# Optimization experiments

Hardware: AMD Instinct MI355X
Metric: run time of the kernel (lower is better)

Reference implementation:

```python
import jax, jax.numpy as jnp
import numpy as np

B, S, CC, CF, E, H, NH = 16, 1024, 8, 8, 64, 1024, 16
DH = H // NH
VOCAB = 10000
EPS = 1e-5


def layer_norm(x, g, b):
    m = x.mean(-1, keepdims=True)
    v = x.var(-1, keepdims=True)
    return (x - m) / jnp.sqrt(v + EPS) * g + b


def setup_inputs():
    key = jax.random.key(0)
    ks = jax.random.split(key, 30)
    f32 = jnp.float32
    n = lambda k, shp, s=0.02: jax.random.normal(k, shp, f32) * s
    inp = {}
    inp['cate_x'] = jax.random.randint(ks[0], (B, S, CC), 0, VOCAB)
    inp['cont_x'] = jax.random.normal(ks[1], (B, S, CF), f32)
    inp['mask'] = jax.random.randint(ks[2], (B, S), 0, 2)
    # parameters
    inp['emb_table'] = n(ks[3], (VOCAB, E)).at[0].set(0.0)  # padding_idx=0
    inp['cate_W'] = n(ks[4], (CC * E, H)); inp['cate_b'] = jnp.zeros((H,), f32)
    inp['cate_ln_g'] = jnp.ones((H,), f32); inp['cate_ln_b'] = jnp.zeros((H,), f32)
    inp['bn_g'] = jnp.ones((CF,), f32); inp['bn_b'] = jnp.zeros((CF,), f32)
    inp['cont_W'] = n(ks[5], (CF, H)); inp['cont_b'] = jnp.zeros((H,), f32)
    inp['cont_ln_g'] = jnp.ones((H,), f32); inp['cont_ln_b'] = jnp.zeros((H,), f32)
    inp['comb_W'] = n(ks[6], (2 * H, H)); inp['comb_b'] = jnp.zeros((H,), f32)
    inp['comb_ln_g'] = jnp.ones((H,), f32); inp['comb_ln_b'] = jnp.zeros((H,), f32)
    inp['Wq'] = n(ks[7], (H, H)); inp['bq'] = jnp.zeros((H,), f32)
    inp['Wk'] = n(ks[8], (H, H)); inp['bk'] = jnp.zeros((H,), f32)
    inp['Wv'] = n(ks[9], (H, H)); inp['bv'] = jnp.zeros((H,), f32)
    inp['Wo'] = n(ks[10], (H, H)); inp['bo'] = jnp.zeros((H,), f32)
    return inp


def reference(cate_x, cont_x, mask, emb_table, cate_W, cate_b, cate_ln_g, cate_ln_b,
              bn_g, bn_b, cont_W, cont_b, cont_ln_g, cont_ln_b,
              comb_W, comb_b, comb_ln_g, comb_ln_b,
              Wq, bq, Wk, bk, Wv, bv, Wo, bo):
    # categorical path: embed -> flatten cols -> Linear+LN
    cate_emb = emb_table[cate_x].reshape(B, S, CC * E)
    cate_h = layer_norm(cate_emb @ cate_W + cate_b, cate_ln_g, cate_ln_b)
    # continuous path: BatchNorm1d over flattened (B*S, CF) with batch stats
    xf = cont_x.reshape(-1, CF)
    mu = xf.mean(0)
    var = xf.var(0)  # biased, as torch BN normalization
    xn = ((xf - mu) / jnp.sqrt(var + EPS) * bn_g + bn_b).reshape(B, S, CF)
    cont_h = layer_norm(xn @ cont_W + cont_b, cont_ln_g, cont_ln_b)
    # combine: ReLU -> Linear -> LN
    seq = jax.nn.relu(jnp.concatenate([cate_h, cont_h], axis=2))
    x = layer_norm(seq @ comb_W + comb_b, comb_ln_g, comb_ln_b)  # [B,S,H]
    # multi-head attention (dropout is identity in eval)
    Q = (x @ Wq + bq).reshape(B, S, NH, DH)
    K = (x @ Wk + bk).reshape(B, S, NH, DH)
    V = (x @ Wv + bv).reshape(B, S, NH, DH)
    scores = jnp.einsum('bqhd,bkhd->bhqk', Q, K) / np.sqrt(DH).astype(np.float32)
    # faithful to source: mask broadcast over the QUERY axis
    scores = jnp.where(mask[:, None, :, None] == 0, -1e7, scores)
    attn = jax.nn.softmax(scores, axis=-1)
    out = jnp.einsum('bhqk,bkhd->bqhd', attn, V).reshape(B, S, H)
    out = out @ Wo + bo
    return out[:, -1:, -1]  # [B,1]
```

## Files before the change

### kernel.cpp

```cpp
#include <hip/hip_runtime.h>
#include <hip/hip_bf16.h>
#include <math.h>

#define EPS 1e-5f

typedef unsigned short u16;
typedef __attribute__((ext_vector_type(8))) short bf16x8;
typedef __attribute__((ext_vector_type(4))) float f32x4;

__device__ __forceinline__ float b2f(u16 u) {
  union { unsigned int i; float f; } v; v.i = ((unsigned int)u) << 16; return v.f;
}
__device__ __forceinline__ u16 f2b(float f) {
  union { float f; unsigned int i; } v; v.f = f;
  unsigned int r = v.i + 0x7fff + ((v.i >> 16) & 1);
  return (u16)(r >> 16);
}

__device__ __forceinline__ void gload_lds16(const u16* g, u16* l) {
  __builtin_amdgcn_global_load_lds(
      (const __attribute__((address_space(1))) unsigned int*)g,
      (__attribute__((address_space(3))) unsigned int*)l, 16, 0, 0);
}

__global__ __launch_bounds__(256) void prep_k(
    const float* __restrict__ cx, float* __restrict__ part_bn,
    float* __restrict__ outacc, float* __restrict__ Sall,
    const float* __restrict__ emb, u16* __restrict__ embb,
    const float* __restrict__ cate_W, u16* __restrict__ cateWT) {
  __shared__ float shmem[64 * 65];
  const int bid = blockIdx.x, tid = threadIdx.x;

  if (bid == 0) {
    if (tid < 16) outacc[tid] = 0.f;
    for (int i = tid; i < 544; i += 256) Sall[i] = 0.f;
    return;
  }
  if (bid <= 64) {
    int pb = bid - 1;
    int gid = pb * 256 + tid;
    float4 a = ((const float4*)cx)[2 * gid];
    float4 b = ((const float4*)cx)[2 * gid + 1];
    float v[16];
    v[0] = a.x; v[1] = a.y; v[2] = a.z; v[3] = a.w;
    v[4] = b.x; v[5] = b.y; v[6] = b.z; v[7] = b.w;
#pragma unroll
    for (int i = 0; i < 8; ++i) v[8 + i] = v[i] * v[i];
#pragma unroll
    for (int off = 32; off; off >>= 1)
#pragma unroll
      for (int i = 0; i < 16; ++i) v[i] += __shfl_down(v[i], off);
    int l = tid & 63, wv_ = tid >> 6;
    if (l == 0)
#pragma unroll
      for (int i = 0; i < 16; ++i) shmem[wv_ * 16 + i] = v[i];
    __syncthreads();
    if (tid < 16)
      part_bn[pb * 16 + tid] = shmem[tid] + shmem[16 + tid] + shmem[32 + tid] + shmem[48 + tid];
    return;
  }
  if (bid <= 689) {
    int i = (bid - 65) * 256 + tid;
    if (i < 160000) {
      float4 v = ((const float4*)emb)[i];
      ushort4 u; u.x = f2b(v.x); u.y = f2b(v.y); u.z = f2b(v.z); u.w = f2b(v.w);
      ((ushort4*)embb)[i] = u;
    }
    return;
  }
  {
    int local = bid - 690;
    int n0 = (local & 15) * 64, k0 = (local >> 4) * 64;
    int c = tid & 63, r0 = tid >> 6;
#pragma unroll
    for (int i = 0; i < 16; ++i) {
      int r = r0 + i * 4;
      shmem[r * 65 + c] = cate_W[(size_t)(k0 + r) * 1024 + n0 + c];
    }
    __syncthreads();
#pragma unroll
    for (int i = 0; i < 16; ++i) {
      int r = r0 + i * 4;
      cateWT[(size_t)(n0 + r) * 512 + k0 + c] = f2b(shmem[c * 65 + r]);
    }
  }
}

template <int MODE>
__global__ __launch_bounds__(512) void gemm256(
    const u16* __restrict__ A0, const u16* __restrict__ A1,
    const int* __restrict__ idx, const u16* __restrict__ embb,
    const u16* __restrict__ BT, const float* __restrict__ bias,
    u16* __restrict__ C, int K) {
  __shared__ u16 As[2][2][8192];
  __shared__ u16 Bs[2][2][8192];
  __shared__ int sidx[MODE == 1 ? 2048 : 4];
  const int tid = threadIdx.x;
  const int bid = blockIdx.x;
  const int chunk = gridDim.x >> 3;
  const int swz = (bid & 7) * chunk + (bid >> 3);
  const int row0 = (swz >> 2) * 256;
  const int col0 = (swz & 3) * 256;

  const int rr8 = tid >> 3;
  const int p8  = tid & 7;
  const int sl  = p8 ^ (rr8 & 7);

  const int l   = tid & 63;
  const int w   = tid >> 6;
  const int wrh = w >> 2;
  const int wcq = w & 3;
  const int hb  = wcq >> 1;
  const int rbb = (wcq & 1) * 64;
  const int lr  = l & 15;
  const int lk  = l >> 4;

  f32x4 acc[8][4];
#pragma unroll
  for (int m = 0; m < 8; ++m)
#pragma unroll
    for (int n = 0; n < 4; ++n) acc[m][n] = (f32x4){0.f, 0.f, 0.f, 0.f};

  const int nt = K >> 6;
  const int nit = nt >> 1;

  if (MODE == 1) {
    *(int4*)&sidx[tid * 4] = *(const int4*)&idx[row0 * 8 + tid * 4];
    __syncthreads();
  }

  auto stageA = [&](int t, int h) {
    const int k0 = t << 6;
    const int buf = t & 1;
#pragma unroll
    for (int i = 0; i < 2; ++i) {
      const u16* asrc;
      if (MODE == 1) {
        int id = sidx[(h * 128 + i * 64 + rr8) * 8 + (k0 >> 6)];
        asrc = embb + (size_t)id * 64 + sl * 8;
      } else {
        int ar = row0 + h * 128 + i * 64 + rr8;
        const u16* base = (k0 < 1024) ? A0 : A1;
        asrc = base + (size_t)ar * 1024 + (k0 & 1023) + sl * 8;
      }
      gload_lds16(asrc, &As[buf][h][i * 4096 + tid * 8]);
    }
  };
  auto stageB = [&](int t, int h) {
    const int k0 = t << 6;
    const int buf = t & 1;
#pragma unroll
    for (int i = 0; i < 2; ++i) {
      int br = col0 + h * 128 + i * 64 + rr8;
      gload_lds16(BT + (size_t)br * K + k0 + sl * 8,
                  &Bs[buf][h][i * 4096 + tid * 8]);
    }
  };

  bf16x8 bfr[4][2];
  auto loadB = [&](int buf) {
#pragma unroll
    for (int n = 0; n < 4; ++n)
#pragma unroll
      for (int ks = 0; ks < 2; ++ks) {
        int rowb = rbb + n * 16 + lr;
        int ph = (ks * 4 + lk) ^ (lr & 7);
        bfr[n][ks] = *(const bf16x8*)&Bs[buf][hb][rowb * 64 + ph * 8];
      }
  };
  auto loadA = [&](bf16x8 (&af)[2][2], int buf, int q) {
#pragma unroll
    for (int mm = 0; mm < 2; ++mm)
#pragma unroll
      for (int ks = 0; ks < 2; ++ks) {
        int rowa = (q * 2 + mm) * 16 + lr;
        int ph = (ks * 4 + lk) ^ (lr & 7);
        af[mm][ks] = *(const bf16x8*)&As[buf][wrh][rowa * 64 + ph * 8];
      }
  };
  auto mfma_quad = [&](bf16x8 (&af)[2][2], int q) {
    __builtin_amdgcn_s_setprio(1);
#pragma unroll
    for (int ks = 0; ks < 2; ++ks)
#pragma unroll
      for (int mm = 0; mm < 2; ++mm)
#pragma unroll
        for (int n = 0; n < 4; ++n)
          acc[q * 2 + mm][n] = __builtin_amdgcn_mfma_f32_16x16x32_bf16(
              af[mm][ks], bfr[n][ks], acc[q * 2 + mm][n], 0, 0, 0);
    __builtin_amdgcn_s_setprio(0);
  };

  stageA(0, 0); stageA(0, 1);
  stageB(0, 0); stageB(0, 1);
  stageB(1, 0); stageB(1, 1);
  asm volatile("s_waitcnt vmcnt(4)" ::: "memory");
  __builtin_amdgcn_s_barrier();

  for (int it = 0; it < nit; ++it) {
    const int T = it * 2;
    const bool more = (T + 2 < nt);
    bf16x8 af[2][2];

    loadB(0); loadA(af, 0, 0);
    stageA(T + 1, 0);
    __builtin_amdgcn_s_barrier();
    asm volatile("s_waitcnt lgkmcnt(0)" ::: "memory");
    mfma_quad(af, 0);
    __builtin_amdgcn_s_barrier();
    loadA(af, 0, 1);
    stageA(T + 1, 1);
    __builtin_amdgcn_s_barrier();
    asm volatile("s_waitcnt lgkmcnt(0)" ::: "memory");
    mfma_quad(af, 1);
    __builtin_amdgcn_s_barrier();
    loadA(af, 0, 2);
    if (more) stageB(T + 2, 0);
    __builtin_amdgcn_s_barrier();
    asm volatile("s_waitcnt lgkmcnt(0)" ::: "memory");
    mfma_quad(af, 2);
    __builtin_amdgcn_s_barrier();
    loadA(af, 0, 3);
    if (more) stageB(T + 2, 1);
    __builtin_amdgcn_s_barrier();
    asm volatile("s_waitcnt lgkmcnt(0)" ::: "memory");
    mfma_quad(af, 3);
    if (more) asm volatile("s_waitcnt vmcnt(4)" ::: "memory");
    else      asm volatile("s_waitcnt vmcnt(0)" ::: "memory");
    __builtin_amdgcn_s_barrier();

    loadB(1); loadA(af, 1, 0);
    if (more) stageA(T + 2, 0);
    __builtin_amdgcn_s_barrier();
    asm volatile("s_waitcnt lgkmcnt(0)" ::: "memory");
    mfma_quad(af, 0);
    __builtin_amdgcn_s_barrier();
    loadA(af, 1, 1);
    if (more) stageA(T + 2, 1);
    __builtin_amdgcn_s_barrier();
    asm volatile("s_waitcnt lgkmcnt(0)" ::: "memory");
    mfma_quad(af, 1);
    __builtin_amdgcn_s_barrier();
    loadA(af, 1, 2);
    if (more) stageB(T + 3, 0);
    __builtin_amdgcn_s_barrier();
    asm volatile("s_waitcnt lgkmcnt(0)" ::: "memory");
    mfma_quad(af, 2);
    __builtin_amdgcn_s_barrier();
    loadA(af, 1, 3);
    if (more) stageB(T + 3, 1);
    __builtin_amdgcn_s_barrier();
    asm volatile("s_waitcnt lgkmcnt(0)" ::: "memory");
    mfma_quad(af, 3);
    if (it + 1 < nit) {
      asm volatile("s_waitcnt vmcnt(4)" ::: "memory");
      __builtin_amdgcn_s_barrier();
    }
  }

  float bv_[4];
#pragma unroll
  for (int n = 0; n < 4; ++n) bv_[n] = bias[col0 + wcq * 64 + n * 16 + lr];
#pragma unroll
  for (int m = 0; m < 8; ++m) {
#pragma unroll
    for (int n = 0; n < 4; ++n) {
      int cc = col0 + wcq * 64 + n * 16 + lr;
#pragma unroll
      for (int q4 = 0; q4 < 4; ++q4) {
        int rr = row0 + wrh * 128 + m * 16 + lk * 4 + q4;
        C[(size_t)rr * 1024 + cc] = f2b(acc[m][n][q4] + bv_[n]);
      }
    }
  }
}

__device__ __forceinline__ void ln_body(u16* __restrict__ buf,
                                        const float* __restrict__ g,
                                        const float* __restrict__ b, int relu,
                                        int blk, int tid) {
  int lane = tid & 63, wave = tid >> 6;
  size_t row = (size_t)blk * 4 + wave;
  u16* p = buf + row * 1024 + lane * 16;
  uint4 u0 = *(uint4*)p;
  uint4 u1 = *(uint4*)(p + 8);
  float x[16];
#pragma unroll
  for (int i = 0; i < 4; ++i) {
    unsigned int w0 = ((unsigned int*)&u0)[i];
    unsigned int w1 = ((unsigned int*)&u1)[i];
    x[2 * i]     = b2f((u16)(w0 & 0xffff));
    x[2 * i + 1] = b2f((u16)(w0 >> 16));
    x[8 + 2 * i]     = b2f((u16)(w1 & 0xffff));
    x[8 + 2 * i + 1] = b2f((u16)(w1 >> 16));
  }
  float s = 0.f, s2 = 0.f;
#pragma unroll
  for (int i = 0; i < 16; ++i) { s += x[i]; s2 += x[i] * x[i]; }
#pragma unroll
  for (int off = 32; off; off >>= 1) { s += __shfl_xor(s, off); s2 += __shfl_xor(s2, off); }
  float mean = s * (1.f / 1024.f);
  float var = s2 * (1.f / 1024.f) - mean * mean;
  float rs = rsqrtf(var + EPS);
  float y[16];
#pragma unroll
  for (int q = 0; q < 4; ++q) {
    float4 gv = *(const float4*)(g + lane * 16 + q * 4);
    float4 bv = *(const float4*)(b + lane * 16 + q * 4);
    y[4 * q]     = (x[4 * q]     - mean) * rs * gv.x + bv.x;
    y[4 * q + 1] = (x[4 * q + 1] - mean) * rs * gv.y + bv.y;
    y[4 * q + 2] = (x[4 * q + 2] - mean) * rs * gv.z + bv.z;
    y[4 * q + 3] = (x[4 * q + 3] - mean) * rs * gv.w + bv.w;
  }
  if (relu)
#pragma unroll
    for (int i = 0; i < 16; ++i) y[i] = fmaxf(y[i], 0.f);
  uint4 o0, o1;
#pragma unroll
  for (int i = 0; i < 4; ++i) {
    ((unsigned int*)&o0)[i] = (unsigned int)f2b(y[2 * i]) | ((unsigned int)f2b(y[2 * i + 1]) << 16);
    ((unsigned int*)&o1)[i] = (unsigned int)f2b(y[8 + 2 * i]) | ((unsigned int)f2b(y[8 + 2 * i + 1]) << 16);
  }
  *(uint4*)p = o0;
  *(uint4*)(p + 8) = o1;
}

__device__ __forceinline__ void cont_body(const float* __restrict__ cx,
                                          const float* __restrict__ part_bn,
                                          const float* __restrict__ bn_g,
                                          const float* __restrict__ bn_b,
                                          const float* __restrict__ W,
                                          const float* __restrict__ cb,
                                          const float* __restrict__ g,
                                          const float* __restrict__ bb,
                                          u16* __restrict__ out,
                                          int row0, int tid) {
  __shared__ float sp[4][16];
  __shared__ float tt[16];
  __shared__ float ab[2][8];
  __shared__ float xn[8][8];
  __shared__ float rr1[4][8], rr2[4][8];

  if (tid < 64) {
    int f = tid & 15, qd = tid >> 4;
    float s = 0.f;
    for (int j = qd * 16; j < qd * 16 + 16; ++j) s += part_bn[j * 16 + f];
    sp[qd][f] = s;
  }
  __syncthreads();
  if (tid < 16) tt[tid] = sp[0][tid] + sp[1][tid] + sp[2][tid] + sp[3][tid];
  __syncthreads();
  if (tid < 8) {
    float mu = tt[tid] * (1.f / 16384.f);
    float var = tt[8 + tid] * (1.f / 16384.f) - mu * mu;
    float a = rsqrtf(var + EPS) * bn_g[tid];
    ab[0][tid] = a;
    ab[1][tid] = bn_b[tid] - mu * a;
  }
  __syncthreads();
  if (tid < 64) {
    int r = tid >> 3, f = tid & 7;
    xn[r][f] = ab[0][f] * cx[(row0 + r) * 8 + f] + ab[1][f];
  }
  __syncthreads();

  int c = tid * 4;
  float4 cbv = *(const float4*)(cb + c);
  float acc[8][4];
#pragma unroll
  for (int r = 0; r < 8; ++r) {
    acc[r][0] = cbv.x; acc[r][1] = cbv.y; acc[r][2] = cbv.z; acc[r][3] = cbv.w;
  }
  for (int k = 0; k < 8; ++k) {
    float4 w4 = *(const float4*)(W + k * 1024 + c);
#pragma unroll
    for (int r = 0; r < 8; ++r) {
      float xv = xn[r][k];
      acc[r][0] = fmaf(xv, w4.x, acc[r][0]);
      acc[r][1] = fmaf(xv, w4.y, acc[r][1]);
      acc[r][2] = fmaf(xv, w4.z, acc[r][2]);
      acc[r][3] = fmaf(xv, w4.w, acc[r][3]);
    }
  }
  float s1[8], s2[8];
#pragma unroll
  for (int r = 0; r < 8; ++r) {
    s1[r] = acc[r][0] + acc[r][1] + acc[r][2] + acc[r][3];
    s2[r] = acc[r][0] * acc[r][0] + acc[r][1] * acc[r][1] +
            acc[r][2] * acc[r][2] + acc[r][3] * acc[r][3];
  }
#pragma unroll
  for (int off = 32; off; off >>= 1)
#pragma unroll
    for (int r = 0; r < 8; ++r) {
      s1[r] += __shfl_down(s1[r], off);
      s2[r] += __shfl_down(s2[r], off);
    }
  int lane = tid & 63, wv = tid >> 6;
  if (lane == 0)
#pragma unroll
    for (int r = 0; r < 8; ++r) { rr1[wv][r] = s1[r]; rr2[wv][r] = s2[r]; }
  __syncthreads();
  float4 gv = *(const float4*)(g + c);
  float4 bv = *(const float4*)(bb + c);
#pragma unroll
  for (int r = 0; r < 8; ++r) {
    float ss = rr1[0][r] + rr1[1][r] + rr1[2][r] + rr1[3][r];
    float qq = rr2[0][r] + rr2[1][r] + rr2[2][r] + rr2[3][r];
    float mean = ss * (1.f / 1024.f);
    float var = qq * (1.f / 1024.f) - mean * mean;
    float rs = rsqrtf(var + EPS);
    float y0 = fmaxf((acc[r][0] - mean) * rs * gv.x + bv.x, 0.f);
    float y1 = fmaxf((acc[r][1] - mean) * rs * gv.y + bv.y, 0.f);
    float y2 = fmaxf((acc[r][2] - mean) * rs * gv.z + bv.z, 0.f);
    float y3 = fmaxf((acc[r][3] - mean) * rs * gv.w + bv.w, 0.f);
    ushort4 o; o.x = f2b(y0); o.y = f2b(y1); o.z = f2b(y2); o.w = f2b(y3);
    *(ushort4*)(out + (size_t)(row0 + r) * 1024 + c) = o;
  }
}

__global__ __launch_bounds__(256) void mid_k(
    u16* __restrict__ X1, const float* __restrict__ cate_g,
    const float* __restrict__ cate_bb,
    const float* __restrict__ comb_W, u16* __restrict__ combWT,
    const float* __restrict__ Wv, const float* __restrict__ Wo,
    const float* __restrict__ comb_g, const float* __restrict__ comb_bbv,
    u16* __restrict__ wvob_hi, u16* __restrict__ wvob_lo,
    float* __restrict__ woc, float* __restrict__ Swg, float* __restrict__ Swb,
    const float* __restrict__ cx, const float* __restrict__ part_bn,
    const float* __restrict__ bn_g, const float* __restrict__ bn_b,
    const float* __restrict__ cont_W, const float* __restrict__ cont_b,
    const float* __restrict__ cont_g, const float* __restrict__ cont_bb,
    u16* __restrict__ X2) {
  __shared__ float shmem[64 * 65];
  const int bid = blockIdx.x, tid = threadIdx.x;
  if (bid < 4096) {
    ln_body(X1, cate_g, cate_bb, 1, bid, tid);
    return;
  }
  if (bid < 4608) {
    int local = bid - 4096;
    int n0 = (local & 15) * 64, k0 = (local >> 4) * 64;
    int c = tid & 63, r0 = tid >> 6;
#pragma unroll
    for (int i = 0; i < 16; ++i) {
      int r = r0 + i * 4;
      shmem[r * 65 + c] = comb_W[(size_t)(k0 + r) * 1024 + n0 + c];
    }
    __syncthreads();
#pragma unroll
    for (int i = 0; i < 16; ++i) {
      int r = r0 + i * 4;
      combWT[(size_t)(n0 + r) * 2048 + k0 + c] = f2b(shmem[c * 65 + r]);
    }
    return;
  }
  if (bid < 4672) {
    int local = bid - 4608;
    int h = local >> 2, jc = local & 3;
    if (tid < 64) shmem[tid] = Wo[(size_t)(h * 64 + tid) * 1024 + 1023];
    __syncthreads();
    if (jc == 0 && tid < 64) woc[h * 64 + tid] = shmem[tid];
    int j = jc * 256 + tid;
    const float* vr = Wv + (size_t)j * 1024 + h * 64;
    float s = 0.f;
    for (int d4 = 0; d4 < 64; d4 += 4) {
      float4 w4 = *(const float4*)(vr + d4);
      s = fmaf(w4.x, shmem[d4], s);
      s = fmaf(w4.y, shmem[d4 + 1], s);
      s = fmaf(w4.z, shmem[d4 + 2], s);
      s = fmaf(w4.w, shmem[d4 + 3], s);
    }
    float sg_ = s * comb_g[j];
    u16 hi = f2b(sg_);
    float lo = sg_ - b2f(hi);
    wvob_hi[h * 1024 + j] = hi;
    wvob_lo[h * 1024 + j] = f2b(lo);
    float swgp = sg_;
    float swbp = s * comb_bbv[j];
#pragma unroll
    for (int off = 32; off; off >>= 1) {
      swgp += __shfl_down(swgp, off);
      swbp += __shfl_down(swbp, off);
    }
    int lane = tid & 63, wv = tid >> 6;
    if (lane == 0) { shmem[64 + wv] = swgp; shmem[68 + wv] = swbp; }
    __syncthreads();
    if (tid == 0) {
      atomicAdd(&Swg[h], shmem[64] + shmem[65] + shmem[66] + shmem[67]);
      atomicAdd(&Swb[h], shmem[68] + shmem[69] + shmem[70] + shmem[71]);
    }
    return;
  }
  {
    int row0 = (bid - 4672) * 8;
    cont_body(cx, part_bn, bn_g, bn_b, cont_W, cont_b, cont_g, cont_bb, X2,
              row0, tid);
  }
}

__global__ __launch_bounds__(256) void qproj_k(const u16* __restrict__ x,
                                               const float* __restrict__ g,
                                               const float* __restrict__ bb,
                                               const float* __restrict__ Wq,
                                               const float* __restrict__ bq,
                                               float* __restrict__ q) {
  __shared__ u16 xs[16][1024];
  __shared__ float part[16][16][16];
  __shared__ float ps1[16][16], ps2[16][16];
  __shared__ float sm[16], sr[16];
  int tid = threadIdx.x;
  for (int i = tid; i < 4096; i += 256) {
    int b = i >> 8, off = (i & 255) * 4;
    *(ushort4*)&xs[b][off] =
        *(const ushort4*)(x + ((size_t)(b * 1024 + 1023)) * 1024 + off);
  }
  __syncthreads();
  {
    int b = tid >> 4, seg = tid & 15;
    float s = 0.f, s2 = 0.f;
    for (int k = seg * 64; k < seg * 64 + 64; ++k) {
      float v = b2f(xs[b][k]);
      s += v;
      s2 = fmaf(v, v, s2);
    }
    ps1[b][seg] = s;
    ps2[b][seg] = s2;
  }
  __syncthreads();
  if (tid < 16) {
    float s = 0.f, s2 = 0.f;
#pragma unroll
    for (int j = 0; j < 16; ++j) { s += ps1[tid][j]; s2 += ps2[tid][j]; }
    float mean = s * (1.f / 1024.f);
    float var = s2 * (1.f / 1024.f) - mean * mean;
    sm[tid] = mean;
    sr[tid] = rsqrtf(var + EPS);
  }
  __syncthreads();
  for (int i = tid; i < 4096; i += 256) {
    int b = i >> 8, off = (i & 255) * 4;
    ushort4 u = *(ushort4*)&xs[b][off];
    float4 gv = *(const float4*)(g + off);
    float4 bv = *(const float4*)(bb + off);
    float m = sm[b], r = sr[b];
    ushort4 o;
    o.x = f2b((b2f(u.x) - m) * r * gv.x + bv.x);
    o.y = f2b((b2f(u.y) - m) * r * gv.y + bv.y);
    o.z = f2b((b2f(u.z) - m) * r * gv.z + bv.z);
    o.w = f2b((b2f(u.w) - m) * r * gv.w + bv.w);
    *(ushort4*)&xs[b][off] = o;
  }
  __syncthreads();
  int c = tid & 15;
  int col = blockIdx.x * 16 + c;
  int kq = tid >> 4;
  float acc[16];
#pragma unroll
  for (int b = 0; b < 16; ++b) acc[b] = 0.f;
  for (int k = kq * 64; k < kq * 64 + 64; ++k) {
    float wv = Wq[(size_t)k * 1024 + col];
#pragma unroll
    for (int b = 0; b < 16; ++b) acc[b] = fmaf(b2f(xs[b][k]), wv, acc[b]);
  }
#pragma unroll
  for (int b = 0; b < 16; ++b) part[kq][b][c] = acc[b];
  __syncthreads();
  {
    int b = tid >> 4, cc = tid & 15;
    float s = 0.f;
#pragma unroll
    for (int j = 0; j < 16; ++j) s += part[j][b][cc];
    q[b * 1024 + blockIdx.x * 16 + cc] = s + bq[blockIdx.x * 16 + cc];
  }
}

__global__ __launch_bounds__(256) void kq_k(const float* __restrict__ Wk,
                                            const float* __restrict__ bk,
                                            const float* __restrict__ q,
                                            const float* __restrict__ g,
                                            const float* __restrict__ bb,
                                            u16* __restrict__ qtb,
                                            float* __restrict__ bkq,
                                            float* __restrict__ Sg,
                                            float* __restrict__ Sb) {
  int h = blockIdx.x >> 2, jc = blockIdx.x & 3;
  int tid = threadIdx.x;
  __shared__ float Qs[16][64];
  __shared__ float rg[4][16], rb[4][16];
  for (int i = tid; i < 1024; i += 256) {
    int b = i >> 6, d = i & 63;
    Qs[b][d] = q[b * 1024 + h * 64 + d];
  }
  __syncthreads();
  int j = jc * 256 + tid;
  float acc[16];
#pragma unroll
  for (int b = 0; b < 16; ++b) acc[b] = 0.f;
  const float* wr = Wk + (size_t)j * 1024 + h * 64;
  for (int d4 = 0; d4 < 64; d4 += 4) {
    float4 w4 = *(const float4*)(wr + d4);
#pragma unroll
    for (int b = 0; b < 16; ++b) {
      acc[b] = fmaf(w4.x, Qs[b][d4], acc[b]);
      acc[b] = fmaf(w4.y, Qs[b][d4 + 1], acc[b]);
      acc[b] = fmaf(w4.z, Qs[b][d4 + 2], acc[b]);
      acc[b] = fmaf(w4.w, Qs[b][d4 + 3], acc[b]);
    }
  }
  float gj = g[j], bbj = bb[j];
  float sgp[16], sbp[16];
#pragma unroll
  for (int b = 0; b < 16; ++b) {
    u16 qg = f2b(acc[b] * gj);
    qtb[((size_t)b * 16 + h) * 1024 + j] = qg;
    sgp[b] = b2f(qg);
    sbp[b] = acc[b] * bbj;
  }
#pragma unroll
  for (int off = 32; off; off >>= 1)
#pragma unroll
    for (int b = 0; b < 16; ++b) {
      sgp[b] += __shfl_down(sgp[b], off);
      sbp[b] += __shfl_down(sbp[b], off);
    }
  int lane = tid & 63, wv = tid >> 6;
  if (lane == 0)
#pragma unroll
    for (int b = 0; b < 16; ++b) { rg[wv][b] = sgp[b]; rb[wv][b] = sbp[b]; }
  __syncthreads();
  if (tid < 16) {
    int b = tid;
    atomicAdd(&Sg[b * 16 + h], rg[0][b] + rg[1][b] + rg[2][b] + rg[3][b]);
    atomicAdd(&Sb[b * 16 + h], rb[0][b] + rb[1][b] + rb[2][b] + rb[3][b]);
  }
  if (jc == 0 && tid < 16) {
    int b = tid;
    float s = 0.f;
    for (int d = 0; d < 64; ++d) s = fmaf(bk[h * 64 + d], Qs[b][d], s);
    bkq[b * 16 + h] = s;
  }
}

__global__ __launch_bounds__(256) void score_k(
    const u16* __restrict__ x, const u16* __restrict__ qtb,
    const float* __restrict__ bkq, const int* __restrict__ mask,
    const u16* __restrict__ whi, const u16* __restrict__ wlo,
    const float* __restrict__ Sg, const float* __restrict__ Sb,
    const float* __restrict__ Swg, const float* __restrict__ Swb,
    float* __restrict__ sc, float* __restrict__ y) {
  int b = blockIdx.x >> 4, kc = blockIdx.x & 15;
  int tid = threadIdx.x;
  int l = tid & 63, w = tid >> 6;
  int keybase = kc * 64 + w * 16;
  int lr = l & 15, ls = l >> 4;
  int masked = (mask[b * 1024 + 1023] == 0);

  bf16x8 ones;
#pragma unroll
  for (int j = 0; j < 8; ++j) ones[j] = (short)0x3F80;

  f32x4 acc = (f32x4){0.f, 0.f, 0.f, 0.f};
  f32x4 acy = (f32x4){0.f, 0.f, 0.f, 0.f};
  f32x4 as1 = (f32x4){0.f, 0.f, 0.f, 0.f};
  f32x4 as2 = (f32x4){0.f, 0.f, 0.f, 0.f};
  const u16* xb = x + (size_t)b * 1024 * 1024;
  const u16* qb = qtb + (size_t)b * 16 * 1024;
  for (int k0 = 0; k0 < 1024; k0 += 32) {
    bf16x8 bfr = *(const bf16x8*)&qb[(size_t)lr * 1024 + k0 + ls * 8];
    bf16x8 bh  = *(const bf16x8*)&whi[(size_t)lr * 1024 + k0 + ls * 8];
    bf16x8 bl  = *(const bf16x8*)&wlo[(size_t)lr * 1024 + k0 + ls * 8];
    bf16x8 afr = *(const bf16x8*)&xb[(size_t)(keybase + lr) * 1024 + k0 + ls * 8];
    acc = __builtin_amdgcn_mfma_f32_16x16x32_bf16(afr, bfr, acc, 0, 0, 0);
    acy = __builtin_amdgcn_mfma_f32_16x16x32_bf16(afr, bh, acy, 0, 0, 0);
    acy = __builtin_amdgcn_mfma_f32_16x16x32_bf16(afr, bl, acy, 0, 0, 0);
    as1 = __builtin_amdgcn_mfma_f32_16x16x32_bf16(afr, ones, as1, 0, 0, 0);
    as2 = __builtin_amdgcn_mfma_f32_16x16x32_bf16(afr, afr, as2, 0, 0, 0);
  }
  int h = lr;
  float bq_  = bkq[b * 16 + h];
  float Sgv  = Sg[b * 16 + h];
  float Sbv  = Sb[b * 16 + h];
  float Swgv = Swg[h];
  float Swbv = Swb[h];
#pragma unroll
  for (int q = 0; q < 4; ++q) {
    int key = keybase + ls * 4 + q;
    float s1 = as1[q];
    float s2 = __shfl(as2[q], ls * 4 + q + 16 * ls);
    float mean = s1 * (1.f / 1024.f);
    float var  = s2 * (1.f / 1024.f) - mean * mean;
    float rs   = rsqrtf(var + EPS);
    float sraw = rs * acc[q] - rs * mean * Sgv + Sbv + bq_;
    float v = masked ? 0.f : sraw * 0.125f;
    sc[((size_t)b * 16 + h) * 1024 + key] = v;
    y[((size_t)b * 16 + h) * 1024 + key] =
        rs * acy[q] - rs * mean * Swgv + Swbv;
  }
}

__global__ __launch_bounds__(256) void fin_k(const float* __restrict__ sc,
                                             const float* __restrict__ y,
                                             float* __restrict__ outacc) {
  int bh = blockIdx.x, tid = threadIdx.x;
  float4 v = ((const float4*)(sc + (size_t)bh * 1024))[tid];
  float m = fmaxf(fmaxf(v.x, v.y), fmaxf(v.z, v.w));
#pragma unroll
  for (int off = 32; off; off >>= 1) m = fmaxf(m, __shfl_down(m, off));
  __shared__ float rm[4], rs_[4], rd_[4];
  int lane = tid & 63, wv = tid >> 6;
  if (lane == 0) rm[wv] = m;
  __syncthreads();
  m = fmaxf(fmaxf(rm[0], rm[1]), fmaxf(rm[2], rm[3]));
  float e0 = expf(v.x - m), e1 = expf(v.y - m), e2 = expf(v.z - m), e3 = expf(v.w - m);
  float4 yv = ((const float4*)(y + (size_t)bh * 1024))[tid];
  float s = e0 + e1 + e2 + e3;
  float d = e0 * yv.x + e1 * yv.y + e2 * yv.z + e3 * yv.w;
#pragma unroll
  for (int off = 32; off; off >>= 1) {
    s += __shfl_down(s, off);
    d += __shfl_down(d, off);
  }
  if (lane == 0) { rs_[wv] = s; rd_[wv] = d; }
  __syncthreads();
  if (tid == 0) {
    float Z = rs_[0] + rs_[1] + rs_[2] + rs_[3];
    float D = rd_[0] + rd_[1] + rd_[2] + rd_[3];
    atomicAdd(&outacc[bh >> 4], D / Z);
  }
}

__global__ __launch_bounds__(256) void bfinal_k(const float* __restrict__ outacc,
                                                const float* __restrict__ bv,
                                                const float* __restrict__ woc,
                                                const float* __restrict__ bo,
                                                float* __restrict__ out) {
  int tid = threadIdx.x;
  float s = 0.f;
  for (int i = tid; i < 1024; i += 256) s = fmaf(bv[i], woc[i], s);
#pragma unroll
  for (int off = 32; off; off >>= 1) s += __shfl_down(s, off);
  __shared__ float r[4];
  int lane = tid & 63, wv = tid >> 6;
  if (lane == 0) r[wv] = s;
  __syncthreads();
  float bc = r[0] + r[1] + r[2] + r[3] + bo[1023];
  if (tid < 16) out[tid] = outacc[tid] + bc;
}

extern "C" void kernel_launch(void* const* d_in, const int* in_sizes, int n_in,
                              void* d_out, int out_size, void* d_ws, size_t ws_size,
                              hipStream_t stream) {
  const int*   cate_x  = (const int*)d_in[0];
  const float* cont_x  = (const float*)d_in[1];
  const int*   mask    = (const int*)d_in[2];
  const float* emb     = (const float*)d_in[3];
  const float* cate_W  = (const float*)d_in[4];
  const float* cate_b  = (const float*)d_in[5];
  const float* cate_g  = (const float*)d_in[6];
  const float* cate_bb = (const float*)d_in[7];
  const float* bn_g    = (const float*)d_in[8];
  const float* bn_b    = (const float*)d_in[9];
  const float* cont_W  = (const float*)d_in[10];
  const float* cont_b  = (const float*)d_in[11];
  const float* cont_g  = (const float*)d_in[12];
  const float* cont_bb = (const float*)d_in[13];
  const float* Wq = (const float*)d_in[18]; const float* bq = (const float*)d_in[19];
  const float* Wk = (const float*)d_in[20]; const float* bk = (const float*)d_in[21];
  const float* Wv = (const float*)d_in[22]; const float* bv = (const float*)d_in[23];
  const float* Wo = (const float*)d_in[24]; const float* bo = (const float*)d_in[25];
  const float* comb_W  = (const float*)d_in[14];
  const float* comb_b  = (const float*)d_in[15];
  const float* comb_g  = (const float*)d_in[16];
  const float* comb_bb = (const float*)d_in[17];
  float* out = (float*)d_out;

  char* w = (char*)d_ws;
  float* stats0  = (float*)w;
  float* outacc  = stats0 + 16;
  float* part_bn = (float*)(w + 256);
  float* qbuf    = (float*)(w + 8192);
  u16* embb      = (u16*)(w + 131328);
  u16* cateWT    = (u16*)(w + 1411328);
  u16* combWT    = (u16*)(w + 2459904);
  float* sc      = (float*)(w + 6654208);
  u16*   qtb     = (u16*)(w + 7702784);
  float* bkq     = (float*)(w + 8292608);
  float* ybuf    = (float*)(w + 8388608);
  u16* wvob_hi   = (u16*)(w + 9437184);
  u16* wvob_lo   = (u16*)(w + 9469952);
  float* woc     = (float*)(w + 9502720);
  float* Sall    = (float*)(w + 10162176);
  float* Sg      = Sall;
  float* Sb      = Sall + 256;
  float* Swg     = Sall + 512;
  float* Swb     = Sall + 528;
  u16* X1        = (u16*)(w + 10848512);
  u16* X2        = X1 + (size_t)16777216;
  u16* xb        = X2 + (size_t)16777216;

  prep_k<<<818, 256, 0, stream>>>(cont_x, part_bn, outacc, Sall, emb, embb,
                                  cate_W, cateWT);

  gemm256<1><<<256, 512, 0, stream>>>(nullptr, nullptr, cate_x, embb, cateWT,
                                      cate_b, X1, 512);
  mid_k<<<6720, 256, 0, stream>>>(X1, cate_g, cate_bb, comb_W, combWT, Wv, Wo,
                                  comb_g, comb_bb, wvob_hi, wvob_lo, woc, Swg,
                                  Swb, cont_x, part_bn, bn_g, bn_b, cont_W,
                                  cont_b, cont_g, cont_bb, X2);
  gemm256<2><<<256, 512, 0, stream>>>(X1, X2, nullptr, nullptr, combWT,
                                      comb_b, xb, 2048);

  qproj_k<<<64, 256, 0, stream>>>(xb, comb_g, comb_bb, Wq, bq, qbuf);
  kq_k<<<64, 256, 0, stream>>>(Wk, bk, qbuf, comb_g, comb_bb, qtb, bkq, Sg, Sb);
  score_k<<<256, 256, 0, stream>>>(xb, qtb, bkq, mask, wvob_hi, wvob_lo,
                                   Sg, Sb, Swg, Swb, sc, ybuf);
  fin_k<<<256, 256, 0, stream>>>(sc, ybuf, outacc);
  bfinal_k<<<1, 256, 0, stream>>>(outacc, bv, woc, bo, out);
}
```

Measured before the change: 189.5 us.

## Split qproj and score reductions across more blocks and fold bias-final into fin_k

The q projection now runs on 256 blocks, each covering a quarter of K, and writes partial sums that kq_k adds together. score_k now uses 1024 blocks, each handling 16 keys with the 1024-long reduction split across four waves, which combine their results through shared memory. The bfinal_k launch is removed: its bias constant is computed in an extra mid_k block and added in fin_k, which accumulates directly into the zeroed output. The aim is better GPU occupancy on the tail kernels and one fewer launch, at the cost of extra partial-sum traffic and an LDS reduction.

```diff
diff --git a/kernel.cpp b/kernel.cpp
--- a/kernel.cpp
+++ b/kernel.cpp
@@ -25,14 +25,14 @@
 
 __global__ __launch_bounds__(256) void prep_k(
     const float* __restrict__ cx, float* __restrict__ part_bn,
-    float* __restrict__ outacc, float* __restrict__ Sall,
+    float* __restrict__ out, float* __restrict__ Sall,
     const float* __restrict__ emb, u16* __restrict__ embb,
     const float* __restrict__ cate_W, u16* __restrict__ cateWT) {
   __shared__ float shmem[64 * 65];
   const int bid = blockIdx.x, tid = threadIdx.x;
 
   if (bid == 0) {
-    if (tid < 16) outacc[tid] = 0.f;
+    if (tid < 16) out[tid] = 0.f;
     for (int i = tid; i < 544; i += 256) Sall[i] = 0.f;
     return;
   }
@@ -426,7 +426,9 @@
     const float* __restrict__ Wv, const float* __restrict__ Wo,
     const float* __restrict__ comb_g, const float* __restrict__ comb_bbv,
     u16* __restrict__ wvob_hi, u16* __restrict__ wvob_lo,
-    float* __restrict__ woc, float* __restrict__ Swg, float* __restrict__ Swb,
+    float* __restrict__ Swg, float* __restrict__ Swb,
+    const float* __restrict__ bv, const float* __restrict__ bo,
+    float* __restrict__ bc,
     const float* __restrict__ cx, const float* __restrict__ part_bn,
     const float* __restrict__ bn_g, const float* __restrict__ bn_b,
     const float* __restrict__ cont_W, const float* __restrict__ cont_b,
@@ -460,7 +462,6 @@
     int h = local >> 2, jc = local & 3;
     if (tid < 64) shmem[tid] = Wo[(size_t)(h * 64 + tid) * 1024 + 1023];
     __syncthreads();
-    if (jc == 0 && tid < 64) woc[h * 64 + tid] = shmem[tid];
     int j = jc * 256 + tid;
     const float* vr = Wv + (size_t)j * 1024 + h * 64;
     float s = 0.f;
@@ -492,10 +493,22 @@
     }
     return;
   }
-  {
+  if (bid < 6720) {
     int row0 = (bid - 4672) * 8;
     cont_body(cx, part_bn, bn_g, bn_b, cont_W, cont_b, cont_g, cont_bb, X2,
               row0, tid);
+    return;
+  }
+  {
+    float s = 0.f;
+    for (int i = tid; i < 1024; i += 256)
+      s = fmaf(bv[i], Wo[(size_t)i * 1024 + 1023], s);
+#pragma unroll
+    for (int off = 32; off; off >>= 1) s += __shfl_down(s, off);
+    int lane = tid & 63, wv = tid >> 6;
+    if (lane == 0) shmem[wv] = s;
+    __syncthreads();
+    if (tid == 0) bc[0] = shmem[0] + shmem[1] + shmem[2] + shmem[3] + bo[1023];
   }
 }
 
@@ -504,12 +517,13 @@
                                                const float* __restrict__ bb,
                                                const float* __restrict__ Wq,
                                                const float* __restrict__ bq,
-                                               float* __restrict__ q) {
+                                               float* __restrict__ qpart) {
   __shared__ u16 xs[16][1024];
   __shared__ float part[16][16][16];
   __shared__ float ps1[16][16], ps2[16][16];
   __shared__ float sm[16], sr[16];
   int tid = threadIdx.x;
+  int cb = blockIdx.x >> 2, kq4 = blockIdx.x & 3;
   for (int i = tid; i < 4096; i += 256) {
     int b = i >> 8, off = (i & 255) * 4;
     *(ushort4*)&xs[b][off] =
@@ -542,23 +556,24 @@
     int b = i >> 8, off = (i & 255) * 4;
     ushort4 u = *(ushort4*)&xs[b][off];
     float4 gv = *(const float4*)(g + off);
-    float4 bv = *(const float4*)(bb + off);
+    float4 bvv = *(const float4*)(bb + off);
     float m = sm[b], r = sr[b];
     ushort4 o;
-    o.x = f2b((b2f(u.x) - m) * r * gv.x + bv.x);
-    o.y = f2b((b2f(u.y) - m) * r * gv.y + bv.y);
-    o.z = f2b((b2f(u.z) - m) * r * gv.z + bv.z);
-    o.w = f2b((b2f(u.w) - m) * r * gv.w + bv.w);
+    o.x = f2b((b2f(u.x) - m) * r * gv.x + bvv.x);
+    o.y = f2b((b2f(u.y) - m) * r * gv.y + bvv.y);
+    o.z = f2b((b2f(u.z) - m) * r * gv.z + bvv.z);
+    o.w = f2b((b2f(u.w) - m) * r * gv.w + bvv.w);
     *(ushort4*)&xs[b][off] = o;
   }
   __syncthreads();
   int c = tid & 15;
-  int col = blockIdx.x * 16 + c;
+  int col = cb * 16 + c;
   int kq = tid >> 4;
   float acc[16];
 #pragma unroll
   for (int b = 0; b < 16; ++b) acc[b] = 0.f;
-  for (int k = kq * 64; k < kq * 64 + 64; ++k) {
+  int kbase = kq4 * 256 + kq * 16;
+  for (int k = kbase; k < kbase + 16; ++k) {
     float wv = Wq[(size_t)k * 1024 + col];
 #pragma unroll
     for (int b = 0; b < 16; ++b) acc[b] = fmaf(b2f(xs[b][k]), wv, acc[b]);
@@ -571,13 +586,14 @@
     float s = 0.f;
 #pragma unroll
     for (int j = 0; j < 16; ++j) s += part[j][b][cc];
-    q[b * 1024 + blockIdx.x * 16 + cc] = s + bq[blockIdx.x * 16 + cc];
+    if (kq4 == 0) s += bq[cb * 16 + cc];
+    qpart[kq4 * 16384 + b * 1024 + cb * 16 + cc] = s;
   }
 }
 
 __global__ __launch_bounds__(256) void kq_k(const float* __restrict__ Wk,
                                             const float* __restrict__ bk,
-                                            const float* __restrict__ q,
+                                            const float* __restrict__ qpart,
                                             const float* __restrict__ g,
                                             const float* __restrict__ bb,
                                             u16* __restrict__ qtb,
@@ -590,7 +606,8 @@
   __shared__ float rg[4][16], rb[4][16];
   for (int i = tid; i < 1024; i += 256) {
     int b = i >> 6, d = i & 63;
-    Qs[b][d] = q[b * 1024 + h * 64 + d];
+    int o = b * 1024 + h * 64 + d;
+    Qs[b][d] = qpart[o] + qpart[16384 + o] + qpart[32768 + o] + qpart[49152 + o];
   }
   __syncthreads();
   int j = jc * 256 + tid;
@@ -649,10 +666,10 @@
     const float* __restrict__ Sg, const float* __restrict__ Sb,
     const float* __restrict__ Swg, const float* __restrict__ Swb,
     float* __restrict__ sc, float* __restrict__ y) {
-  int b = blockIdx.x >> 4, kc = blockIdx.x & 15;
+  int b = blockIdx.x >> 6, kg = blockIdx.x & 63;
   int tid = threadIdx.x;
   int l = tid & 63, w = tid >> 6;
-  int keybase = kc * 64 + w * 16;
+  int keybase = kg * 16;
   int lr = l & 15, ls = l >> 4;
   int masked = (mask[b * 1024 + 1023] == 0);
 
@@ -666,7 +683,8 @@
   f32x4 as2 = (f32x4){0.f, 0.f, 0.f, 0.f};
   const u16* xb = x + (size_t)b * 1024 * 1024;
   const u16* qb = qtb + (size_t)b * 16 * 1024;
-  for (int k0 = 0; k0 < 1024; k0 += 32) {
+  const int k0beg = w * 256;
+  for (int k0 = k0beg; k0 < k0beg + 256; k0 += 32) {
     bf16x8 bfr = *(const bf16x8*)&qb[(size_t)lr * 1024 + k0 + ls * 8];
     bf16x8 bh  = *(const bf16x8*)&whi[(size_t)lr * 1024 + k0 + ls * 8];
     bf16x8 bl  = *(const bf16x8*)&wlo[(size_t)lr * 1024 + k0 + ls * 8];
@@ -677,31 +695,52 @@
     as1 = __builtin_amdgcn_mfma_f32_16x16x32_bf16(afr, ones, as1, 0, 0, 0);
     as2 = __builtin_amdgcn_mfma_f32_16x16x32_bf16(afr, afr, as2, 0, 0, 0);
   }
-  int h = lr;
-  float bq_  = bkq[b * 16 + h];
-  float Sgv  = Sg[b * 16 + h];
-  float Sbv  = Sb[b * 16 + h];
-  float Swgv = Swg[h];
-  float Swbv = Swb[h];
-#pragma unroll
-  for (int q = 0; q < 4; ++q) {
-    int key = keybase + ls * 4 + q;
-    float s1 = as1[q];
-    float s2 = __shfl(as2[q], ls * 4 + q + 16 * ls);
-    float mean = s1 * (1.f / 1024.f);
-    float var  = s2 * (1.f / 1024.f) - mean * mean;
-    float rs   = rsqrtf(var + EPS);
-    float sraw = rs * acc[q] - rs * mean * Sgv + Sbv + bq_;
-    float v = masked ? 0.f : sraw * 0.125f;
-    sc[((size_t)b * 16 + h) * 1024 + key] = v;
-    y[((size_t)b * 16 + h) * 1024 + key] =
-        rs * acy[q] - rs * mean * Swgv + Swbv;
+
+  __shared__ float red[3][64][16];
+  if (w > 0) {
+    float* r = red[w - 1][l];
+#pragma unroll
+    for (int q = 0; q < 4; ++q) {
+      r[q] = acc[q]; r[4 + q] = acy[q]; r[8 + q] = as1[q]; r[12 + q] = as2[q];
+    }
+  }
+  __syncthreads();
+  if (w == 0) {
+#pragma unroll
+    for (int i = 0; i < 3; ++i) {
+      const float* r = red[i][l];
+#pragma unroll
+      for (int q = 0; q < 4; ++q) {
+        acc[q] += r[q]; acy[q] += r[4 + q]; as1[q] += r[8 + q]; as2[q] += r[12 + q];
+      }
+    }
+    int h = lr;
+    float bq_  = bkq[b * 16 + h];
+    float Sgv  = Sg[b * 16 + h];
+    float Sbv  = Sb[b * 16 + h];
+    float Swgv = Swg[h];
+    float Swbv = Swb[h];
+#pragma unroll
+    for (int q = 0; q < 4; ++q) {
+      int key = keybase + ls * 4 + q;
+      float s1 = as1[q];
+      float s2 = __shfl(as2[q], ls * 4 + q + 16 * ls);
+      float mean = s1 * (1.f / 1024.f);
+      float var  = s2 * (1.f / 1024.f) - mean * mean;
+      float rs   = rsqrtf(var + EPS);
+      float sraw = rs * acc[q] - rs * mean * Sgv + Sbv + bq_;
+      float v = masked ? 0.f : sraw * 0.125f;
+      sc[((size_t)b * 16 + h) * 1024 + key] = v;
+      y[((size_t)b * 16 + h) * 1024 + key] =
+          rs * acy[q] - rs * mean * Swgv + Swbv;
+    }
   }
 }
 
 __global__ __launch_bounds__(256) void fin_k(const float* __restrict__ sc,
                                              const float* __restrict__ y,
-                                             float* __restrict__ outacc) {
+                                             const float* __restrict__ bc,
+                                             float* __restrict__ out) {
   int bh = blockIdx.x, tid = threadIdx.x;
   float4 v = ((const float4*)(sc + (size_t)bh * 1024))[tid];
   float m = fmaxf(fmaxf(v.x, v.y), fmaxf(v.z, v.w));
@@ -726,26 +765,10 @@
   if (tid == 0) {
     float Z = rs_[0] + rs_[1] + rs_[2] + rs_[3];
     float D = rd_[0] + rd_[1] + rd_[2] + rd_[3];
-    atomicAdd(&outacc[bh >> 4], D / Z);
-  }
-}
-
-__global__ __launch_bounds__(256) void bfinal_k(const float* __restrict__ outacc,
-                                                const float* __restrict__ bv,
-                                                const float* __restrict__ woc,
-                                                const float* __restrict__ bo,
-                                                float* __restrict__ out) {
-  int tid = threadIdx.x;
-  float s = 0.f;
-  for (int i = tid; i < 1024; i += 256) s = fmaf(bv[i], woc[i], s);
-#pragma unroll
-  for (int off = 32; off; off >>= 1) s += __shfl_down(s, off);
-  __shared__ float r[4];
-  int lane = tid & 63, wv = tid >> 6;
-  if (lane == 0) r[wv] = s;
-  __syncthreads();
-  float bc = r[0] + r[1] + r[2] + r[3] + bo[1023];
-  if (tid < 16) out[tid] = outacc[tid] + bc;
+    float add = D / Z;
+    if ((bh & 15) == 0) add += bc[0];
+    atomicAdd(&out[bh >> 4], add);
+  }
 }
 
 extern "C" void kernel_launch(void* const* d_in, const int* in_sizes, int n_in,
@@ -776,10 +799,7 @@
   float* out = (float*)d_out;
 
   char* w = (char*)d_ws;
-  float* stats0  = (float*)w;
-  float* outacc  = stats0 + 16;
   float* part_bn = (float*)(w + 256);
-  float* qbuf    = (float*)(w + 8192);
   u16* embb      = (u16*)(w + 131328);
   u16* cateWT    = (u16*)(w + 1411328);
   u16* combWT    = (u16*)(w + 2459904);
@@ -789,32 +809,32 @@
   float* ybuf    = (float*)(w + 8388608);
   u16* wvob_hi   = (u16*)(w + 9437184);
   u16* wvob_lo   = (u16*)(w + 9469952);
-  float* woc     = (float*)(w + 9502720);
+  float* qpart   = (float*)(w + 9506816);
   float* Sall    = (float*)(w + 10162176);
   float* Sg      = Sall;
   float* Sb      = Sall + 256;
   float* Swg     = Sall + 512;
   float* Swb     = Sall + 528;
+  float* bc      = Sall + 552;
   u16* X1        = (u16*)(w + 10848512);
   u16* X2        = X1 + (size_t)16777216;
   u16* xb        = X2 + (size_t)16777216;
 
-  prep_k<<<818, 256, 0, stream>>>(cont_x, part_bn, outacc, Sall, emb, embb,
+  prep_k<<<818, 256, 0, stream>>>(cont_x, part_bn, out, Sall, emb, embb,
                                   cate_W, cateWT);
 
   gemm256<1><<<256, 512, 0, stream>>>(nullptr, nullptr, cate_x, embb, cateWT,
                                       cate_b, X1, 512);
-  mid_k<<<6720, 256, 0, stream>>>(X1, cate_g, cate_bb, comb_W, combWT, Wv, Wo,
-                                  comb_g, comb_bb, wvob_hi, wvob_lo, woc, Swg,
-                                  Swb, cont_x, part_bn, bn_g, bn_b, cont_W,
-                                  cont_b, cont_g, cont_bb, X2);
+  mid_k<<<6721, 256, 0, stream>>>(X1, cate_g, cate_bb, comb_W, combWT, Wv, Wo,
+                                  comb_g, comb_bb, wvob_hi, wvob_lo, Swg, Swb,
+                                  bv, bo, bc, cont_x, part_bn, bn_g, bn_b,
+                                  cont_W, cont_b, cont_g, cont_bb, X2);
   gemm256<2><<<256, 512, 0, stream>>>(X1, X2, nullptr, nullptr, combWT,
                                       comb_b, xb, 2048);
 
-  qproj_k<<<64, 256, 0, stream>>>(xb, comb_g, comb_bb, Wq, bq, qbuf);
-  kq_k<<<64, 256, 0, stream>>>(Wk, bk, qbuf, comb_g, comb_bb, qtb, bkq, Sg, Sb);
-  score_k<<<256, 256, 0, stream>>>(xb, qtb, bkq, mask, wvob_hi, wvob_lo,
-                                   Sg, Sb, Swg, Swb, sc, ybuf);
-  fin_k<<<256, 256, 0, stream>>>(sc, ybuf, outacc);
-  bfinal_k<<<1, 256, 0, stream>>>(outacc, bv, woc, bo, out);
-}
+  qproj_k<<<256, 256, 0, stream>>>(xb, comb_g, comb_bb, Wq, bq, qpart);
+  kq_k<<<64, 256, 0, stream>>>(Wk, bk, qpart, comb_g, comb_bb, qtb, bkq, Sg, Sb);
+  score_k<<<1024, 256, 0, stream>>>(xb, qtb, bkq, mask, wvob_hi, wvob_lo,
+                                    Sg, Sb, Swg, Swb, sc, ybuf);
+  fin_k<<<256, 256, 0, stream>>>(sc, ybuf, bc, out);
+}
```

After: 181.5 us (median of 2 runs). -4.2%, faster.
